# Optimization experiments

Hardware: AMD Instinct MI355X
Metric: run time of the kernel (lower is better)

Reference implementation:

```python
import jax, jax.numpy as jnp
import numpy as np

D = 128          # embedding_size
K = 8            # num_components
S = 65536        # seq_len
SCALE = 1.0 / np.sqrt(2.0 * np.pi)  # keeps det(2*pi*Sigma) and exp(-maha/2) in fp32 range


def setup_inputs() -> dict:
    key = jax.random.key(0)
    kx, kw, kb = jax.random.split(key, 3)
    x = jax.random.normal(kx, (1, S, D), dtype=jnp.float32) * SCALE
    W = jax.random.normal(kw, (D, K), dtype=jnp.float32) / np.sqrt(D)
    b = jax.random.normal(kb, (K,), dtype=jnp.float32) * 0.01
    return {"x": x, "W": W, "b": b}


def reference(x, W, b):
    xs = x[0]                                    # [S, D]  (x.squeeze())
    seq_len = xs.shape[0]
    # component responsibilities: Linear + Softmax
    gamma = jax.nn.softmax(xs @ W + b, axis=-1)  # [S, K]
    Nk = jnp.sum(gamma, axis=0)                  # [K]   sum of component weights
    phi = Nk / seq_len                           # [K]   mixture weights (component_weight_)
    # per-component means: sum_j gamma_jk x_j / Nk
    mu = (gamma.T @ xs) / Nk[:, None]            # [K, D]
    diff = xs[:, None, :] - mu[None, :, :]       # [S, K, D]
    # per-component covariance: sum_j gamma_jk (x_j-mu_k)(x_j-mu_k)^T / Nk
    sigma = jnp.einsum('sk,skd,ske->kde', gamma, diff, diff) / Nk[:, None, None]  # [K, D, D]
    inv_sigma = jnp.linalg.inv(sigma)            # [K, D, D]
    # Mahalanobis distance per (sample, component)
    maha = jnp.einsum('skd,kde,ske->sk', diff, inv_sigma, diff)  # [S, K]
    two_pi = jnp.float32(2.0 * np.pi)
    det = jnp.abs(jnp.linalg.det(two_pi * sigma))                # [K]  det(2*pi*Sigma_k)
    dens = jnp.sum(phi * jnp.exp(-0.5 * maha) / jnp.sqrt(det), axis=-1)  # [S]
    energy = -jnp.sum(jnp.log(dens))
    return energy.reshape(1, 1)
```

## Files before the change

### kernel.cpp

```cpp
#include <hip/hip_runtime.h>


#define S_LEN 65536
#define D 128
#define K 8
#define NCH 32
#define KSTEP 64
#define NXTCH (S_LEN / KSTEP)
#define MB_S 128
#define NMB (S_LEN / MB_S)

#define OFF_GT 0
#define SZ_GT (NXTCH * K * KSTEP)
#define OFF_M2P (OFF_GT + SZ_GT)
#define SZ_M2P (K * NCH * D * D)
#define OFF_MSP (OFF_M2P + SZ_M2P)
#define SZ_MSP (K * NCH * D)
#define OFF_NKP (OFF_MSP + SZ_MSP)
#define SZ_NKP (K * NCH)
#define OFF_NK (OFF_NKP + SZ_NKP)
#define OFF_MU (OFF_NK + 8)
#define OFF_SIGMA (OFF_MU + K * D)
#define OFF_WV (OFF_SIGMA + K * D * D)
#define OFF_COEF (OFF_WV + K * D)
#define OFF_C2 (OFF_COEF + 8)
#define OFF_EPART (OFF_C2 + 8)
#define OFF_XB (OFF_EPART + NMB)
#define SZ_XB (S_LEN * D / 2)
#define OFF_XT (OFF_XB + SZ_XB)
#define SZ_XT (S_LEN * D / 2)
#define OFF_BH (OFF_XT + SZ_XT)

#define LOG_2PI 1.8378770664093453f

typedef __attribute__((ext_vector_type(8))) short short8;
typedef __attribute__((ext_vector_type(4))) float f32x4;

__device__ __forceinline__ float bflo(unsigned u) { return __uint_as_float(u << 16); }
__device__ __forceinline__ float bfhi(unsigned u) { return __uint_as_float(u & 0xffff0000u); }
__device__ __forceinline__ unsigned packbf(float a, float b) {
  unsigned ua = __float_as_uint(a); ua = ua + 0x7fffu + ((ua >> 16) & 1);
  unsigned ub = __float_as_uint(b); ub = ub + 0x7fffu + ((ub >> 16) & 1);
  return (ua >> 16) | (ub & 0xffff0000u);
}
__device__ __forceinline__ unsigned short f2bf(float a) {
  unsigned ua = __float_as_uint(a); ua = ua + 0x7fffu + ((ua >> 16) & 1);
  return (unsigned short)(ua >> 16);
}

__global__ __launch_bounds__(256) void k_gamma(const float* __restrict__ x,
                                               const float* __restrict__ W,
                                               const float* __restrict__ b,
                                               float* __restrict__ gt) {
  __shared__ float Wt[K][D];
  __shared__ float bl[K];
  int tid = threadIdx.x;
  for (int it = 0; it < 4; ++it) {
    int idx = it * 256 + tid;
    Wt[idx & 7][idx >> 3] = W[idx];
  }
  if (tid < K) bl[tid] = b[tid];
  __syncthreads();

  int s = blockIdx.x * 256 + tid;
  float li[K];
#pragma unroll
  for (int k = 0; k < K; ++k) li[k] = bl[k];
  const float4* xr = (const float4*)(x + (size_t)s * D);
#pragma unroll 8
  for (int i = 0; i < 32; ++i) {
    float4 xv = xr[i];
#pragma unroll
    for (int k = 0; k < K; ++k) {
      float4 wv = *(const float4*)&Wt[k][i * 4];
      li[k] += xv.x * wv.x + xv.y * wv.y + xv.z * wv.z + xv.w * wv.w;
    }
  }
  float m = li[0];
#pragma unroll
  for (int k = 1; k < K; ++k) m = fmaxf(m, li[k]);
  float p[K];
  float sum = 0.f;
#pragma unroll
  for (int k = 0; k < K; ++k) { p[k] = expf(li[k] - m); sum += p[k]; }
  float inv = 1.0f / sum;
  int ch = s >> 6, sl = s & 63;
#pragma unroll
  for (int k = 0; k < K; ++k) gt[(size_t)ch * (K * 64) + k * 64 + sl] = p[k] * inv;
}

__global__ __launch_bounds__(256) void k_xprep(const float* __restrict__ x,
                                               unsigned short* __restrict__ xb,
                                               unsigned short* __restrict__ xt) {
  __shared__ unsigned short xr[64 * 136];
  int tid = threadIdx.x;
  for (int c = 0; c < 4; ++c) {
    int sb = blockIdx.x * 256 + c * 64;
    if (c) __syncthreads();
    {
      int s = tid >> 2, db = (tid & 3) * 32;
      const float4* src = (const float4*)(x + (size_t)(sb + s) * D + db);
#pragma unroll
      for (int j = 0; j < 4; ++j) {
        float4 v0 = src[j * 2], v1 = src[j * 2 + 1];
        unsigned u0 = packbf(v0.x, v0.y), u1 = packbf(v0.z, v0.w);
        unsigned u2 = packbf(v1.x, v1.y), u3 = packbf(v1.z, v1.w);
        uint4 o = {u0, u1, u2, u3};
        *(uint4*)&xr[s * 136 + db + j * 8] = o;
      }
    }
    __syncthreads();
    {
      int s = tid >> 2, u0 = (tid & 3) * 4;
      uint4* dst = (uint4*)(xb + (size_t)(sb + s) * D) + u0;
#pragma unroll
      for (int j = 0; j < 4; ++j) dst[j] = *(const uint4*)&xr[s * 136 + (u0 + j) * 8];
    }
    {
      int d = tid >> 1, lu0 = (tid & 1) * 4;
      uint4* dst = (uint4*)(xt + (size_t)(sb >> 6) * (D * 64) + d * 64) + lu0;
#pragma unroll
      for (int j = 0; j < 4; ++j) {
        int s0 = (lu0 + j) * 8;
        unsigned w[4];
#pragma unroll
        for (int q = 0; q < 4; ++q) {
          unsigned lo = xr[(s0 + 2 * q) * 136 + d];
          unsigned hi = xr[(s0 + 2 * q + 1) * 136 + d];
          w[q] = lo | (hi << 16);
        }
        uint4 o = {w[0], w[1], w[2], w[3]};
        dst[j] = o;
      }
    }
  }
}

__global__ __launch_bounds__(256) void k_m2(const unsigned short* __restrict__ xt,
                                            const float* __restrict__ gt,
                                            float* __restrict__ m2p,
                                            float* __restrict__ msp,
                                            float* __restrict__ nkp) {
  __shared__ unsigned short zt[D * 64];
  __shared__ float gbuf[2][64], sgbuf[2][64];
  __shared__ float msred[256];
  int tid = threadIdx.x;
  int cblk = blockIdx.x, k = blockIdx.y;
  int ch0 = cblk * 32;

  int w = tid >> 6;
  int m0 = (w >> 1) * 64, n0 = (w & 1) * 64;
  int lg = (tid >> 4) & 3, ll = tid & 15;

  const uint4* xtg = (const uint4*)xt;
  uint4 xr[4];
  {
    const uint4* src = xtg + (size_t)ch0 * 1024 + tid * 4;
#pragma unroll
    for (int j = 0; j < 4; ++j) xr[j] = src[j];
  }
  float gacc = 0.f, gn = 0.f;
  if (tid < 64) {
    float g0 = gt[(size_t)ch0 * (K * 64) + k * 64 + tid];
    gbuf[0][tid] = g0; sgbuf[0][tid] = sqrtf(g0); gacc = g0;
    gn = gt[(size_t)(ch0 + 1) * (K * 64) + k * 64 + tid];
  }
  __syncthreads();

  f32x4 acc[4][4];
#pragma unroll
  for (int mi = 0; mi < 4; ++mi)
#pragma unroll
    for (int ni = 0; ni < 4; ++ni) acc[mi][ni] = (f32x4)0.f;

  float msa = 0.f;
  int dloc = tid >> 1;

  for (int t = 0; t < 32; ++t) {
    int cur = t & 1;
#pragma unroll
    for (int j = 0; j < 4; ++j) {
      int lu = (tid & 1) * 4 + j, s0 = lu * 8;
      uint4 q = xr[j];
      float x0 = bflo(q.x), x1 = bfhi(q.x), x2 = bflo(q.y), x3 = bfhi(q.y);
      float x4 = bflo(q.z), x5 = bfhi(q.z), x6 = bflo(q.w), x7 = bfhi(q.w);
      float4 g0 = *(const float4*)&gbuf[cur][s0];
      float4 g1 = *(const float4*)&gbuf[cur][s0 + 4];
      float4 s0v = *(const float4*)&sgbuf[cur][s0];
      float4 s1v = *(const float4*)&sgbuf[cur][s0 + 4];
      msa += x0 * g0.x + x1 * g0.y + x2 * g0.z + x3 * g0.w +
             x4 * g1.x + x5 * g1.y + x6 * g1.z + x7 * g1.w;
      unsigned u0 = packbf(x0 * s0v.x, x1 * s0v.y);
      unsigned u1 = packbf(x2 * s0v.z, x3 * s0v.w);
      unsigned u2 = packbf(x4 * s1v.x, x5 * s1v.y);
      unsigned u3 = packbf(x6 * s1v.z, x7 * s1v.w);
      uint4 o = {u0, u1, u2, u3};
      *(uint4*)&zt[dloc * 64 + (lu ^ (dloc & 7)) * 8] = o;
    }
    if (tid < 64 && t + 1 < 32) {
      gbuf[cur ^ 1][tid] = gn; sgbuf[cur ^ 1][tid] = sqrtf(gn); gacc += gn;
    }
    if (t + 1 < 32) {
      const uint4* src = xtg + (size_t)(ch0 + t + 1) * 1024 + tid * 4;
#pragma unroll
      for (int j = 0; j < 4; ++j) xr[j] = src[j];
      if (tid < 64 && t + 2 < 32)
        gn = gt[(size_t)(ch0 + t + 2) * (K * 64) + k * 64 + tid];
    }
    __syncthreads();
#pragma unroll
    for (int ksub = 0; ksub < 2; ++ksub) {
      short8 af[4], bf_[4];
#pragma unroll
      for (int mi = 0; mi < 4; ++mi) {
        int dd = m0 + mi * 16 + ll;
        int ua = ksub * 4 + lg;
        af[mi] = *(const short8*)&zt[dd * 64 + (ua ^ (dd & 7)) * 8];
      }
#pragma unroll
      for (int ni = 0; ni < 4; ++ni) {
        int ee = n0 + ni * 16 + ll;
        int ub = ksub * 4 + lg;
        bf_[ni] = *(const short8*)&zt[ee * 64 + (ub ^ (ee & 7)) * 8];
      }
#pragma unroll
      for (int mi = 0; mi < 4; ++mi)
#pragma unroll
        for (int ni = 0; ni < 4; ++ni)
          acc[mi][ni] = __builtin_amdgcn_mfma_f32_16x16x32_bf16(
              af[mi], bf_[ni], acc[mi][ni], 0, 0, 0);
    }
    __syncthreads();
  }

  size_t base = (size_t)(k * NCH + cblk) << 14;
#pragma unroll
  for (int mi = 0; mi < 4; ++mi)
#pragma unroll
    for (int ni = 0; ni < 4; ++ni)
#pragma unroll
      for (int r = 0; r < 4; ++r) {
        int row = m0 + mi * 16 + lg * 4 + r;
        int col = n0 + ni * 16 + ll;
        m2p[base + row * D + col] = acc[mi][ni][r];
      }
  msred[tid] = msa;
  __syncthreads();
  if (tid < 128) msp[(size_t)(k * NCH + cblk) * D + tid] = msred[2 * tid] + msred[2 * tid + 1];
  if (tid < 64) {
    float v = gacc;
#pragma unroll
    for (int off = 1; off < 64; off <<= 1) v += __shfl_xor(v, off);
    if (tid == 0) nkp[k * NCH + cblk] = v;
  }
}

__global__ __launch_bounds__(256) void k_redmu(const float* __restrict__ msp,
                                               const float* __restrict__ nkp,
                                               float* __restrict__ Nk,
                                               float* __restrict__ mu) {
  __shared__ float sNk[K];
  int tid = threadIdx.x;
  if (tid < K) {
    float s = 0.f;
    for (int c = 0; c < NCH; ++c) s += nkp[tid * NCH + c];
    sNk[tid] = s;
    Nk[tid] = s;
  }
  __syncthreads();
  for (int it = 0; it < (K * D) / 256; ++it) {
    int idx = it * 256 + tid;
    int k = idx >> 7;
    float s = 0.f;
    for (int c = 0; c < NCH; ++c) s += msp[(size_t)(k * NCH + c) * D + (idx & 127)];
    mu[idx] = s / sNk[k];
  }
}

__global__ __launch_bounds__(256) void k_sigma(const float* __restrict__ m2p,
                                               const float* __restrict__ Nk,
                                               const float* __restrict__ mu,
                                               float* __restrict__ sigma) {
  int tid = threadIdx.x;
  int k = blockIdx.y;
  int flat = blockIdx.x * 256 + tid;
  int d = flat >> 7, e = flat & 127;
  float s = 0.f;
  for (int c = 0; c < NCH; ++c) s += m2p[((size_t)(k * NCH + c) << 14) + flat];
  sigma[((size_t)k << 14) + flat] = s / Nk[k] - mu[k * D + d] * mu[k * D + e];
}

#define PBW 36
#define YTW 132
#define AROT(r, c) (((r) << 7) + ((((c) + (((r) >> 3) << 2))) & 127))

__global__ __launch_bounds__(256) void k_inv(const float* __restrict__ sigma,
                                             const float* __restrict__ Nk,
                                             const float* __restrict__ mu,
                                             unsigned short* __restrict__ Bh,
                                             float* __restrict__ vv,
                                             float* __restrict__ coef,
                                             float* __restrict__ c2) {
  __shared__ float A[D * D];
  __shared__ float Pb[32 * PBW];
  __shared__ float Cb[32 * 128];
  __shared__ float Yt[32 * YTW];
  __shared__ float Rb[32 * 128];
  __shared__ float mus[D];
  int tid = threadIdx.x;
  int k = blockIdx.x;
  const float* sg = sigma + ((size_t)k << 14);

#pragma unroll
  for (int i = 0; i < 16; ++i) {
    int f = tid + 256 * i;
    int r = f >> 5, c4 = (f & 31) << 2;
    *(float4*)&A[AROT(r, c4)] = *(const float4*)&sg[((size_t)f) << 2];
  }
  if (tid < D) mus[tid] = mu[k * D + tid];
  __syncthreads();

  float ldet = 0.f;
  int mr = tid >> 3, mq = tid & 7;
  int ci = tid >> 1, ch = tid & 1;
  int w = tid >> 6, l = tid & 63;
  int d0 = (((w >> 1) << 3) + (l >> 3)) * 8;
  int e0 = (((w & 1) << 3) + (l & 7)) * 8;

  for (int t = 0; t < 4; ++t) {
    int tb = t * 32;
    *(float4*)&Pb[mr * PBW + 4 * mq] = *(const float4*)&A[AROT(tb + mr, tb + 4 * mq)];
#pragma unroll
    for (int q = 0; q < 4; ++q) {
      int f = tid + 256 * q;
      int rr = f >> 5, cc4 = (f & 31) << 2;
      *(float4*)&Rb[rr * 128 + cc4] = *(const float4*)&A[AROT(tb + rr, cc4)];
    }
#pragma unroll
    for (int n4 = 0; n4 < 4; ++n4) {
      float4 q4 = *(const float4*)&A[AROT(ci, tb + 16 * ch + 4 * n4)];
      int nb = 16 * ch + 4 * n4;
      Cb[(nb + 0) * 128 + ci] = q4.x;
      Cb[(nb + 1) * 128 + ci] = q4.y;
      Cb[(nb + 2) * 128 + ci] = q4.z;
      Cb[(nb + 3) * 128 + ci] = q4.w;
    }
    __syncthreads();

    for (int c = 0; c < 32; ++c) {
      float dpv = Pb[c * PBW + c];
      float piv = 1.0f / dpv;
      ldet += logf(dpv);
      float4 rq = *(const float4*)&Pb[c * PBW + 4 * mq];
      float cv = Pb[mr * PBW + c];
      __syncthreads();
      float4 rfac = {piv * rq.x, piv * rq.y, piv * rq.z, piv * rq.w};
      float4 own = *(const float4*)&Pb[mr * PBW + 4 * mq];
      bool pr = (mr == c);
      float4 up;
      up.x = pr ? rfac.x : own.x - cv * rfac.x;
      up.y = pr ? rfac.y : own.y - cv * rfac.y;
      up.z = pr ? rfac.z : own.z - cv * rfac.z;
      up.w = pr ? rfac.w : own.w - cv * rfac.w;
      int cq = c >> 2, cl = c & 3;
      if (mq == cq) {
        float nv = pr ? -piv : cv * piv;
        if (cl == 0) up.x = nv;
        else if (cl == 1) up.y = nv;
        else if (cl == 2) up.z = nv;
        else up.w = nv;
      }
      *(float4*)&Pb[mr * PBW + 4 * mq] = up;
      __syncthreads();
    }

    {
      int rs = tid >> 3, cs = tid & 7;
      float accY[4][4] = {};
#pragma unroll 8
      for (int n = 0; n < 32; ++n) {
        float4 cq4 = *(const float4*)&Cb[n * 128 + 4 * rs];
        float4 pq = *(const float4*)&Pb[n * PBW + 4 * cs];
        float ca[4] = {cq4.x, cq4.y, cq4.z, cq4.w};
        float pa[4] = {pq.x, pq.y, pq.z, pq.w};
#pragma unroll
        for (int q = 0; q < 4; ++q)
#pragma unroll
          for (int j = 0; j < 4; ++j) accY[q][j] -= ca[q] * pa[j];
      }
#pragma unroll
      for (int j = 0; j < 4; ++j) {
        float4 o = {accY[0][j], accY[1][j], accY[2][j], accY[3][j]};
        *(float4*)&Yt[(4 * cs + j) * YTW + 4 * rs] = o;
      }
    }
    __syncthreads();

    {
      float acc[8][8];
#pragma unroll
      for (int di = 0; di < 8; ++di)
#pragma unroll
        for (int e4 = 0; e4 < 2; ++e4) {
          float4 a = *(const float4*)&A[AROT(d0 + di, e0 + 4 * e4)];
          acc[di][e4 * 4 + 0] = a.x; acc[di][e4 * 4 + 1] = a.y;
          acc[di][e4 * 4 + 2] = a.z; acc[di][e4 * 4 + 3] = a.w;
        }
#pragma unroll 4
      for (int m = 0; m < 32; ++m) {
        float4 ya = *(const float4*)&Yt[m * YTW + d0];
        float4 yb = *(const float4*)&Yt[m * YTW + d0 + 4];
        float4 ra = *(const float4*)&Rb[m * 128 + e0];
        float4 rb2 = *(const float4*)&Rb[m * 128 + e0 + 4];
        float av[8] = {ya.x, ya.y, ya.z, ya.w, yb.x, yb.y, yb.z, yb.w};
        float bv[8] = {ra.x, ra.y, ra.z, ra.w, rb2.x, rb2.y, rb2.z, rb2.w};
#pragma unroll
        for (int di = 0; di < 8; ++di)
#pragma unroll
          for (int ei = 0; ei < 8; ++ei) acc[di][ei] -= av[di] * bv[ei];
      }
#pragma unroll
      for (int di = 0; di < 8; ++di)
#pragma unroll
        for (int e4 = 0; e4 < 2; ++e4) {
          float4 o = {acc[di][e4 * 4 + 0], acc[di][e4 * 4 + 1],
                      acc[di][e4 * 4 + 2], acc[di][e4 * 4 + 3]};
          *(float4*)&A[AROT(d0 + di, e0 + 4 * e4)] = o;
        }
    }
    __syncthreads();

#pragma unroll
    for (int qq = 0; qq < 4; ++qq) {
      int j0 = 4 * mq + 32 * qq;
      *(float4*)&A[AROT(tb + mr, j0)] = *(const float4*)&Yt[mr * YTW + j0];
    }
    if (ci < tb || ci >= tb + 32) {
#pragma unroll
      for (int n = 0; n < 16; ++n) {
        int mloc = 16 * ch + ((n + ci) & 15);
        A[AROT(ci, tb + mloc)] = Yt[mloc * YTW + ci];
      }
    }
    __syncthreads();
    *(float4*)&A[AROT(tb + mr, tb + 4 * mq)] = *(const float4*)&Pb[mr * PBW + 4 * mq];
    __syncthreads();
  }

#pragma unroll
  for (int i = 0; i < 16; ++i) {
    int f = tid + 256 * i;
    int r = f >> 5, c4 = (f & 31) << 2;
    float4 a = *(const float4*)&A[AROT(r, c4)];
    unsigned u0 = packbf(-a.x, -a.y), u1 = packbf(-a.z, -a.w);
    uint2 o = {u0, u1};
    *(uint2*)(Bh + (size_t)k * (D * D) + f * 4) = o;
  }
  float c2part = 0.f;
  if (tid < D) {
    float s = 0.f;
#pragma unroll 8
    for (int q = 0; q < 32; ++q) {
      float4 a = *(const float4*)&A[AROT(tid, q << 2)];
      float4 m = *(const float4*)&mus[q << 2];
      s += a.x * m.x + a.y * m.y + a.z * m.z + a.w * m.w;
    }
    vv[k * D + tid] = -s;
    c2part = mus[tid] * (-s);
  }
  __syncthreads();
  {
    float v = c2part;
#pragma unroll
    for (int off = 1; off < 64; off <<= 1) v += __shfl_xor(v, off);
    if ((tid & 63) == 0) Pb[tid >> 6] = v;
  }
  __syncthreads();
  if (tid == 0) {
    c2[k] = Pb[0] + Pb[1];
    coef[k] = logf(Nk[k] * (1.0f / (float)S_LEN)) -
              0.5f * ((float)D * LOG_2PI + ldet);
  }
}

__global__ __launch_bounds__(256) void k_maha(const unsigned short* __restrict__ xb,
                                              const unsigned short* __restrict__ Bh,
                                              const float* __restrict__ vv,
                                              const float* __restrict__ coef,
                                              const float* __restrict__ c2,
                                              float* __restrict__ epart) {
  __shared__ unsigned short xbt[MB_S * D];
  __shared__ unsigned short Bt[D * 64];
  __shared__ float vls[K * D];
  __shared__ float cfl[K], c2l[K];
  __shared__ float wsum[4];
  int tid = threadIdx.x;
  int bs = blockIdx.x * MB_S;
  int w = tid >> 6;
  int m0 = w * 32;
  int lg = (tid >> 4) & 3, ll = tid & 15;

  {
    int s = tid >> 1, u0 = (tid & 1) * 8;
    const uint4* src = (const uint4*)(xb + (size_t)(bs + s) * D) + u0;
#pragma unroll
    for (int j = 0; j < 8; ++j)
      *(uint4*)&xbt[s * D + ((u0 + j) ^ (s & 7)) * 8] = src[j];
  }
#pragma unroll
  for (int i = 0; i < 4; ++i) { int idx = i * 256 + tid; vls[idx] = vv[idx]; }
  if (tid < K) { cfl[tid] = coef[tid]; c2l[tid] = c2[tid]; }

  const uint4* bg = (const uint4*)Bh;
  uint4 br[4];
  {
    int e = tid >> 1, u0b = (tid & 1) * 4;
    const uint4* src = bg + (size_t)0 * 2048 + e * 16 + 0 * 8 + u0b;
#pragma unroll
    for (int j = 0; j < 4; ++j) br[j] = src[j];
  }

  f32x4 acc[2][8];
  float mrun[2][4], srun[2][4];
#pragma unroll
  for (int mi = 0; mi < 2; ++mi)
#pragma unroll
    for (int r = 0; r < 4; ++r) { mrun[mi][r] = -1e30f; srun[mi][r] = 0.f; }

  for (int it = 0; it < 16; ++it) {
    int k = it >> 1, dh = it & 1;
    {
      int e = tid >> 1, lu0 = (tid & 1) * 4;
#pragma unroll
      for (int j = 0; j < 4; ++j)
        *(uint4*)&Bt[e * 64 + ((lu0 + j) ^ (e & 7)) * 8] = br[j];
    }
    if (it < 15) {
      int kn = (it + 1) >> 1, dhn = (it + 1) & 1;
      int e = tid >> 1, u0b = (tid & 1) * 4;
      const uint4* src = bg + (size_t)kn * 2048 + e * 16 + dhn * 8 + u0b;
#pragma unroll
      for (int j = 0; j < 4; ++j) br[j] = src[j];
    }
    if (dh == 0) {
#pragma unroll
      for (int mi = 0; mi < 2; ++mi)
#pragma unroll
        for (int ni = 0; ni < 8; ++ni) acc[mi][ni] = (f32x4)0.f;
    }
    __syncthreads();
#pragma unroll
    for (int ksub = 0; ksub < 2; ++ksub) {
      short8 af[2];
#pragma unroll
      for (int mi = 0; mi < 2; ++mi) {
        int srow = m0 + mi * 16 + ll;
        int ua = dh * 8 + ksub * 4 + lg;
        af[mi] = *(const short8*)&xbt[srow * D + (ua ^ (srow & 7)) * 8];
      }
#pragma unroll
      for (int ni = 0; ni < 8; ++ni) {
        int e = ni * 16 + ll;
        int ub = ksub * 4 + lg;
        short8 bfr = *(const short8*)&Bt[e * 64 + (ub ^ (e & 7)) * 8];
#pragma unroll
        for (int mi = 0; mi < 2; ++mi)
          acc[mi][ni] = __builtin_amdgcn_mfma_f32_16x16x32_bf16(
              af[mi], bfr, acc[mi][ni], 0, 0, 0);
      }
    }
    if (dh == 1) {
      float part[2][4] = {};
#pragma unroll
      for (int ni = 0; ni < 8; ++ni) {
        int col = ni * 16 + ll;
        float w2 = -2.0f * vls[k * D + col];
#pragma unroll
        for (int mi = 0; mi < 2; ++mi)
#pragma unroll
          for (int r = 0; r < 4; ++r) {
            int srow = m0 + mi * 16 + lg * 4 + r;
            unsigned xv = xbt[srow * D + ((col >> 3) ^ (srow & 7)) * 8 + (col & 7)];
            part[mi][r] += bflo(xv) * (acc[mi][ni][r] + w2);
          }
      }
#pragma unroll
      for (int mi = 0; mi < 2; ++mi)
#pragma unroll
        for (int r = 0; r < 4; ++r) {
          float p = part[mi][r];
          p += __shfl_xor(p, 1); p += __shfl_xor(p, 2);
          p += __shfl_xor(p, 4); p += __shfl_xor(p, 8);
          float a = cfl[k] - 0.5f * (p + c2l[k]);
          if (a > mrun[mi][r]) {
            srun[mi][r] = srun[mi][r] * expf(mrun[mi][r] - a) + 1.0f;
            mrun[mi][r] = a;
          } else {
            srun[mi][r] += expf(a - mrun[mi][r]);
          }
        }
    }
    __syncthreads();
  }

  float v = 0.f;
#pragma unroll
  for (int mi = 0; mi < 2; ++mi)
#pragma unroll
    for (int r = 0; r < 4; ++r) v += mrun[mi][r] + logf(srun[mi][r]);
  v += __shfl_xor(v, 16);
  v += __shfl_xor(v, 32);
  if ((tid & 63) == 0) wsum[w] = v;
  __syncthreads();
  if (tid == 0) epart[blockIdx.x] = wsum[0] + wsum[1] + wsum[2] + wsum[3];
}

__global__ __launch_bounds__(256) void k_final(const float* __restrict__ epart,
                                               float* __restrict__ out) {
  __shared__ double sw[4];
  int tid = threadIdx.x;
  double a = (double)epart[tid] + (double)epart[tid + 256];
#pragma unroll
  for (int off = 1; off < 64; off <<= 1) a += __shfl_xor(a, off);
  if ((tid & 63) == 0) sw[tid >> 6] = a;
  __syncthreads();
  if (tid == 0) out[0] = (float)(-(sw[0] + sw[1] + sw[2] + sw[3]));
}

extern "C" void kernel_launch(void* const* d_in, const int* in_sizes, int n_in,
                              void* d_out, int out_size, void* d_ws, size_t ws_size,
                              hipStream_t stream) {
  (void)in_sizes; (void)n_in; (void)out_size; (void)ws_size;
  const float* x = (const float*)d_in[0];
  const float* W = (const float*)d_in[1];
  const float* b = (const float*)d_in[2];
  float* out = (float*)d_out;
  float* ws = (float*)d_ws;

  float* gtp   = ws + OFF_GT;
  float* m2p   = ws + OFF_M2P;
  float* msp   = ws + OFF_MSP;
  float* nkp   = ws + OFF_NKP;
  float* Nk    = ws + OFF_NK;
  float* mu    = ws + OFF_MU;
  float* sigma = ws + OFF_SIGMA;
  float* wvp   = ws + OFF_WV;
  float* coefp = ws + OFF_COEF;
  float* c2p   = ws + OFF_C2;
  float* epart = ws + OFF_EPART;
  unsigned short* xb = (unsigned short*)(ws + OFF_XB);
  unsigned short* xt = (unsigned short*)(ws + OFF_XT);
  unsigned short* Bh = (unsigned short*)(ws + OFF_BH);

  k_gamma<<<S_LEN / 256, 256, 0, stream>>>(x, W, b, gtp);
  k_xprep<<<S_LEN / 256, 256, 0, stream>>>(x, xb, xt);
  k_m2<<<dim3(NCH, K), 256, 0, stream>>>(xt, gtp, m2p, msp, nkp);
  k_redmu<<<1, 256, 0, stream>>>(msp, nkp, Nk, mu);
  k_sigma<<<dim3(64, K), 256, 0, stream>>>(m2p, Nk, mu, sigma);
  k_inv<<<K, 256, 0, stream>>>(sigma, Nk, mu, Bh, wvp, coefp, c2p);
  k_maha<<<NMB, 256, 0, stream>>>(xb, Bh, wvp, coefp, c2p, epart);
  k_final<<<1, 256, 0, stream>>>(epart, out);
}
```

Before: 337.2 us.

## Keep x tile in registers and stage full per-component B in LDS for k_maha

The Mahalanobis kernel no longer stages the x tile in shared memory. Each lane loads its MFMA A-fragments and the epilogue x values straight from global memory into registers. The per-component B matrix is now staged whole (128x128) in LDS, so the loop runs 8 iterations instead of 16 half-steps, halving the barriers. The online log-sum-exp update becomes branch-free with fmaxf. In exchange, register pressure rises (af, ex and br[8]) and the scattered per-element global loads for ex may be uncoalesced.

```diff
diff --git a/kernel.cpp b/kernel.cpp
--- a/kernel.cpp
+++ b/kernel.cpp
@@ -38,14 +38,11 @@
 
 __device__ __forceinline__ float bflo(unsigned u) { return __uint_as_float(u << 16); }
 __device__ __forceinline__ float bfhi(unsigned u) { return __uint_as_float(u & 0xffff0000u); }
+__device__ __forceinline__ float bfu(unsigned short u) { return __uint_as_float((unsigned)u << 16); }
 __device__ __forceinline__ unsigned packbf(float a, float b) {
   unsigned ua = __float_as_uint(a); ua = ua + 0x7fffu + ((ua >> 16) & 1);
   unsigned ub = __float_as_uint(b); ub = ub + 0x7fffu + ((ub >> 16) & 1);
   return (ua >> 16) | (ub & 0xffff0000u);
-}
-__device__ __forceinline__ unsigned short f2bf(float a) {
-  unsigned ua = __float_as_uint(a); ua = ua + 0x7fffu + ((ua >> 16) & 1);
-  return (unsigned short)(ua >> 16);
 }
 
 __global__ __launch_bounds__(256) void k_gamma(const float* __restrict__ x,
@@ -489,117 +486,105 @@
                                               const float* __restrict__ coef,
                                               const float* __restrict__ c2,
                                               float* __restrict__ epart) {
-  __shared__ unsigned short xbt[MB_S * D];
-  __shared__ unsigned short Bt[D * 64];
+  __shared__ unsigned short Bt[D * D];
   __shared__ float vls[K * D];
   __shared__ float cfl[K], c2l[K];
   __shared__ float wsum[4];
   int tid = threadIdx.x;
   int bs = blockIdx.x * MB_S;
-  int w = tid >> 6;
+  int w = tid >> 6, l = tid & 63;
   int m0 = w * 32;
   int lg = (tid >> 4) & 3, ll = tid & 15;
 
-  {
-    int s = tid >> 1, u0 = (tid & 1) * 8;
-    const uint4* src = (const uint4*)(xb + (size_t)(bs + s) * D) + u0;
-#pragma unroll
-    for (int j = 0; j < 8; ++j)
-      *(uint4*)&xbt[s * D + ((u0 + j) ^ (s & 7)) * 8] = src[j];
-  }
+  short8 af[2][4];
+#pragma unroll
+  for (int mi = 0; mi < 2; ++mi) {
+    const unsigned short* rp = xb + (size_t)(bs + m0 + mi * 16 + ll) * D;
+#pragma unroll
+    for (int jj = 0; jj < 4; ++jj)
+      af[mi][jj] = *(const short8*)(rp + jj * 32 + lg * 8);
+  }
+  unsigned short ex[2][4][8];
+#pragma unroll
+  for (int mi = 0; mi < 2; ++mi)
+#pragma unroll
+    for (int r = 0; r < 4; ++r) {
+      const unsigned short* rp = xb + (size_t)(bs + m0 + mi * 16 + lg * 4 + r) * D + ll;
+#pragma unroll
+      for (int ni = 0; ni < 8; ++ni) ex[mi][r][ni] = rp[ni * 16];
+    }
+
 #pragma unroll
   for (int i = 0; i < 4; ++i) { int idx = i * 256 + tid; vls[idx] = vv[idx]; }
   if (tid < K) { cfl[tid] = coef[tid]; c2l[tid] = c2[tid]; }
 
   const uint4* bg = (const uint4*)Bh;
-  uint4 br[4];
-  {
-    int e = tid >> 1, u0b = (tid & 1) * 4;
-    const uint4* src = bg + (size_t)0 * 2048 + e * 16 + 0 * 8 + u0b;
-#pragma unroll
-    for (int j = 0; j < 4; ++j) br[j] = src[j];
-  }
-
-  f32x4 acc[2][8];
+  uint4 br[8];
+#pragma unroll
+  for (int j = 0; j < 8; ++j) br[j] = bg[j * 256 + tid];
+
   float mrun[2][4], srun[2][4];
 #pragma unroll
   for (int mi = 0; mi < 2; ++mi)
 #pragma unroll
     for (int r = 0; r < 4; ++r) { mrun[mi][r] = -1e30f; srun[mi][r] = 0.f; }
 
-  for (int it = 0; it < 16; ++it) {
-    int k = it >> 1, dh = it & 1;
-    {
-      int e = tid >> 1, lu0 = (tid & 1) * 4;
-#pragma unroll
-      for (int j = 0; j < 4; ++j)
-        *(uint4*)&Bt[e * 64 + ((lu0 + j) ^ (e & 7)) * 8] = br[j];
-    }
-    if (it < 15) {
-      int kn = (it + 1) >> 1, dhn = (it + 1) & 1;
-      int e = tid >> 1, u0b = (tid & 1) * 4;
-      const uint4* src = bg + (size_t)kn * 2048 + e * 16 + dhn * 8 + u0b;
-#pragma unroll
-      for (int j = 0; j < 4; ++j) br[j] = src[j];
-    }
-    if (dh == 0) {
-#pragma unroll
-      for (int mi = 0; mi < 2; ++mi)
-#pragma unroll
-        for (int ni = 0; ni < 8; ++ni) acc[mi][ni] = (f32x4)0.f;
-    }
-    __syncthreads();
-#pragma unroll
-    for (int ksub = 0; ksub < 2; ++ksub) {
-      short8 af[2];
-#pragma unroll
-      for (int mi = 0; mi < 2; ++mi) {
-        int srow = m0 + mi * 16 + ll;
-        int ua = dh * 8 + ksub * 4 + lg;
-        af[mi] = *(const short8*)&xbt[srow * D + (ua ^ (srow & 7)) * 8];
-      }
+  for (int k = 0; k < K; ++k) {
+#pragma unroll
+    for (int j = 0; j < 8; ++j) {
+      int u = j * 256 + tid;
+      int e = u >> 4, du = u & 15;
+      *(uint4*)&Bt[e * D + ((du ^ (e & 7)) << 3)] = br[j];
+    }
+    if (k + 1 < K) {
+      const uint4* src = bg + (size_t)(k + 1) * 2048;
+#pragma unroll
+      for (int j = 0; j < 8; ++j) br[j] = src[j * 256 + tid];
+    }
+    __syncthreads();
+
+    f32x4 acc[2][8];
+#pragma unroll
+    for (int mi = 0; mi < 2; ++mi)
+#pragma unroll
+      for (int ni = 0; ni < 8; ++ni) acc[mi][ni] = (f32x4)0.f;
+#pragma unroll
+    for (int jj = 0; jj < 4; ++jj) {
 #pragma unroll
       for (int ni = 0; ni < 8; ++ni) {
         int e = ni * 16 + ll;
-        int ub = ksub * 4 + lg;
-        short8 bfr = *(const short8*)&Bt[e * 64 + (ub ^ (e & 7)) * 8];
+        int du = jj * 4 + lg;
+        short8 bfr = *(const short8*)&Bt[e * D + ((du ^ (e & 7)) << 3)];
 #pragma unroll
         for (int mi = 0; mi < 2; ++mi)
           acc[mi][ni] = __builtin_amdgcn_mfma_f32_16x16x32_bf16(
-              af[mi], bfr, acc[mi][ni], 0, 0, 0);
-      }
-    }
-    if (dh == 1) {
-      float part[2][4] = {};
-#pragma unroll
-      for (int ni = 0; ni < 8; ++ni) {
-        int col = ni * 16 + ll;
-        float w2 = -2.0f * vls[k * D + col];
-#pragma unroll
-        for (int mi = 0; mi < 2; ++mi)
-#pragma unroll
-          for (int r = 0; r < 4; ++r) {
-            int srow = m0 + mi * 16 + lg * 4 + r;
-            unsigned xv = xbt[srow * D + ((col >> 3) ^ (srow & 7)) * 8 + (col & 7)];
-            part[mi][r] += bflo(xv) * (acc[mi][ni][r] + w2);
-          }
-      }
+              af[mi][jj], bfr, acc[mi][ni], 0, 0, 0);
+      }
+    }
+
+    float part[2][4] = {};
+#pragma unroll
+    for (int ni = 0; ni < 8; ++ni) {
+      int col = ni * 16 + ll;
+      float w2 = -2.0f * vls[k * D + col];
 #pragma unroll
       for (int mi = 0; mi < 2; ++mi)
 #pragma unroll
-        for (int r = 0; r < 4; ++r) {
-          float p = part[mi][r];
-          p += __shfl_xor(p, 1); p += __shfl_xor(p, 2);
-          p += __shfl_xor(p, 4); p += __shfl_xor(p, 8);
-          float a = cfl[k] - 0.5f * (p + c2l[k]);
-          if (a > mrun[mi][r]) {
-            srun[mi][r] = srun[mi][r] * expf(mrun[mi][r] - a) + 1.0f;
-            mrun[mi][r] = a;
-          } else {
-            srun[mi][r] += expf(a - mrun[mi][r]);
-          }
-        }
-    }
+        for (int r = 0; r < 4; ++r)
+          part[mi][r] += bfu(ex[mi][r][ni]) * (acc[mi][ni][r] + w2);
+    }
+#pragma unroll
+    for (int mi = 0; mi < 2; ++mi)
+#pragma unroll
+      for (int r = 0; r < 4; ++r) {
+        float p = part[mi][r];
+        p += __shfl_xor(p, 1); p += __shfl_xor(p, 2);
+        p += __shfl_xor(p, 4); p += __shfl_xor(p, 8);
+        float a = cfl[k] - 0.5f * (p + c2l[k]);
+        float mn = fmaxf(mrun[mi][r], a);
+        srun[mi][r] = srun[mi][r] * expf(mrun[mi][r] - mn) + expf(a - mn);
+        mrun[mi][r] = mn;
+      }
     __syncthreads();
   }
 
@@ -610,7 +595,7 @@
     for (int r = 0; r < 4; ++r) v += mrun[mi][r] + logf(srun[mi][r]);
   v += __shfl_xor(v, 16);
   v += __shfl_xor(v, 32);
-  if ((tid & 63) == 0) wsum[w] = v;
+  if (l == 0) wsum[w] = v;
   __syncthreads();
   if (tid == 0) epart[blockIdx.x] = wsum[0] + wsum[1] + wsum[2] + wsum[3];
 }
```

Measured after the change: 298.7 us. 11.4% less time.
